# Kernel optimization log

Hardware: AMD Instinct MI355X
Metric: run time of the kernel (lower is better)

Reference implementation:

```python
import jax, jax.numpy as jnp
import numpy as np

TOP_P = 0.95        # sample() default topp
TEMPERATURE = 0.8   # token_temperature
NEG_INF = float('-inf')


def setup_inputs() -> dict:
    key = jax.random.key(0)
    k1, k2 = jax.random.split(key)
    B, V = 8192, 2048  # batch rows x speech-unit vocab
    logits = jax.random.normal(k1, (B, V), dtype=jnp.float32) * 4.0
    # uniform noise for Gumbel-max multinomial sampling (open interval)
    u = jax.random.uniform(k2, (B, V), dtype=jnp.float32, minval=1e-6, maxval=1.0 - 1e-6)
    return {"logits": logits, "u": u}


def _top_p_filter(logits, p):
    # descending sort (matches torch.sort(descending=True))
    order = jnp.argsort(-logits, axis=-1)                      # [B, V]
    sorted_logits = jnp.take_along_axis(logits, order, axis=-1)
    cum = jnp.cumsum(jax.nn.softmax(sorted_logits, axis=-1), axis=-1)
    remove = cum > p
    # shift right by one so the first token above the threshold is kept
    remove = jnp.concatenate(
        [jnp.zeros_like(remove[..., :1]), remove[..., :-1]], axis=-1)
    # scatter mask back to unsorted order via inverse permutation
    inv = jnp.argsort(order, axis=-1)
    remove_unsorted = jnp.take_along_axis(remove, inv, axis=-1)
    return jnp.where(remove_unsorted, NEG_INF, logits)


def reference(logits, u):
    scaled = logits / TEMPERATURE
    filtered = _top_p_filter(scaled, TOP_P)                    # [B, V]
    probs = jax.nn.softmax(filtered, axis=-1)                  # [B, V]
    # multinomial(probs, 1) == Gumbel-max over filtered logits
    gumbel = -jnp.log(-jnp.log(u))
    sampled = jnp.argmax(filtered + gumbel, axis=-1, keepdims=True)  # [B, 1]
    return sampled, probs
```

## Files before the change

### kernel.cpp

```cpp
#include <hip/hip_runtime.h>
#include <math.h>

#define VOCAB 2048
#define TPB   256
#define NBINS 64
#define BIN_SCALE 6.0f
#define BCAP  512

typedef float vf4 __attribute__((ext_vector_type(4)));

__device__ __forceinline__ unsigned long long pack_key(float z, int idx) {
    unsigned zb = __float_as_uint(z);
    zb = (zb & 0x80000000u) ? ~zb : (zb | 0x80000000u);
    return ((unsigned long long)zb << 32) | (unsigned)(VOCAB - 1 - idx);
}

__global__ __launch_bounds__(TPB, 8) void sampler_kernel(
    const float* __restrict__ logits,
    const float* __restrict__ uni,
    float* __restrict__ out_idx,
    float* __restrict__ out_probs)
{
    const int row  = blockIdx.x;
    const int t    = threadIdx.x;
    const int lane = t & 63;
    const int wid  = t >> 6;

    __shared__ float  s_bins[NBINS];
    __shared__ float  s_wf[4];
    __shared__ double s_wd[4];
    __shared__ unsigned long long s_key[4];
    __shared__ int    s_cnt;
    __shared__ float  s_cv[BCAP];
    __shared__ float  s_ce[BCAP];

    const float* lrow = logits    + (size_t)row * VOCAB;
    const float* urow = uni       + (size_t)row * VOCAB;
    float*       prow = out_probs + (size_t)row * VOCAB;

    if (t < NBINS) s_bins[t] = 0.0f;
    if (t == 0) s_cnt = 0;

    const vf4 a0 = *(const vf4*)(lrow + 4 * t);
    const vf4 a1 = *(const vf4*)(lrow + VOCAB / 2 + 4 * t);
    float s[8] = {a0.x * 1.25f, a0.y * 1.25f, a0.z * 1.25f, a0.w * 1.25f,
                  a1.x * 1.25f, a1.y * 1.25f, a1.z * 1.25f, a1.w * 1.25f};

    float lm = s[0];
    #pragma unroll
    for (int j = 1; j < 8; j++) lm = fmaxf(lm, s[j]);
    #pragma unroll
    for (int off = 32; off; off >>= 1) lm = fmaxf(lm, __shfl_down(lm, off));
    if (lane == 0) s_wf[wid] = lm;
    __syncthreads();
    const float m = fmaxf(fmaxf(s_wf[0], s_wf[1]), fmaxf(s_wf[2], s_wf[3]));

    float e[8];
    int   bin[8];
    float psum = 0.0f;
    #pragma unroll
    for (int j = 0; j < 8; j++) {
        e[j] = __expf(s[j] - m);
        psum += e[j];
        bin[j] = (int)((m - s[j]) * BIN_SCALE);
        if (bin[j] < NBINS) atomicAdd(&s_bins[bin[j]], e[j]);
    }
    double dp = (double)psum;
    #pragma unroll
    for (int off = 32; off; off >>= 1) dp += __shfl_down(dp, off);
    if (lane == 0) s_wd[wid] = dp;
    __syncthreads();

    const double S  = s_wd[0] + s_wd[1] + s_wd[2] + s_wd[3];
    const double pS = 0.95 * S;
    const float  bf = s_bins[lane];
    double c = (double)bf;
    #pragma unroll
    for (int d = 1; d < 64; d <<= 1) {
        double o = __shfl_up(c, d);
        if (lane >= d) c += o;
    }
    unsigned long long ball = __ballot(c > pS);
    const int    bstar     = ball ? (__ffsll(ball) - 1) : (NBINS - 1);
    const double cumBefore = __shfl(c - (double)bf, bstar);

    #pragma unroll
    for (int j = 0; j < 8; j++) {
        if (bin[j] == bstar) {
            int pos = atomicAdd(&s_cnt, 1);
            if (pos < BCAP) { s_cv[pos] = s[j]; s_ce[pos] = e[j]; }
        }
    }
    __syncthreads();
    const int cnt = min(s_cnt, BCAP);

    float SKb = 0.0f;
    for (int i = 0; i < cnt; i++) {
        float vi = s_cv[i], part = 0.0f;
        for (int jj = 0; jj < cnt; jj++)
            part += (s_cv[jj] > vi) ? s_ce[jj] : 0.0f;
        if (cumBefore + (double)part <= pS) SKb += s_ce[i];
    }
    const float invSK = 1.0f / (float)(cumBefore + (double)SKb);

    unsigned keptMask = 0;
    #pragma unroll
    for (int j = 0; j < 8; j++) {
        bool kept;
        if (bin[j] < bstar)      kept = true;
        else if (bin[j] > bstar) kept = false;
        else {
            float part = 0.0f;
            for (int i = 0; i < cnt; i++)
                part += (s_cv[i] > s[j]) ? s_ce[i] : 0.0f;
            kept = (cumBefore + (double)part) <= pS;
        }
        if (kept) keptMask |= (1u << j);
    }

    vf4 p0, p1;
    p0.x = (keptMask & 0x01) ? e[0] * invSK : 0.0f;
    p0.y = (keptMask & 0x02) ? e[1] * invSK : 0.0f;
    p0.z = (keptMask & 0x04) ? e[2] * invSK : 0.0f;
    p0.w = (keptMask & 0x08) ? e[3] * invSK : 0.0f;
    p1.x = (keptMask & 0x10) ? e[4] * invSK : 0.0f;
    p1.y = (keptMask & 0x20) ? e[5] * invSK : 0.0f;
    p1.z = (keptMask & 0x40) ? e[6] * invSK : 0.0f;
    p1.w = (keptMask & 0x80) ? e[7] * invSK : 0.0f;
    __builtin_nontemporal_store(p0, (vf4*)(prow + 4 * t));
    __builtin_nontemporal_store(p1, (vf4*)(prow + VOCAB / 2 + 4 * t));

    unsigned long long key = 0ull;
    #pragma unroll
    for (int j = 0; j < 8; j++) {
        if ((keptMask >> j) & 1u) {
            int   idx = (j < 4) ? (4 * t + j) : (VOCAB / 2 + 4 * t + (j - 4));
            float uv  = urow[idx];
            float z   = s[j] + (-logf(-logf(uv)));
            unsigned long long kk = pack_key(z, idx);
            key = (kk > key) ? kk : key;
        }
    }
    #pragma unroll
    for (int off = 32; off; off >>= 1) {
        unsigned long long ok = __shfl_down(key, off);
        key = (ok > key) ? ok : key;
    }
    if (lane == 0) s_key[wid] = key;
    __syncthreads();
    if (t == 0) {
        unsigned long long k0 = s_key[0];
        #pragma unroll
        for (int w = 1; w < 4; w++) k0 = (s_key[w] > k0) ? s_key[w] : k0;
        out_idx[row] = (float)(VOCAB - 1 - (int)(k0 & 0xFFFFFFFFu));
    }
}

extern "C" void kernel_launch(void* const* d_in, const int* in_sizes, int n_in,
                              void* d_out, int out_size, void* d_ws, size_t ws_size,
                              hipStream_t stream) {
    const float* logits = (const float*)d_in[0];
    const float* u      = (const float*)d_in[1];
    const int B = in_sizes[0] / VOCAB;
    float* out_idx   = (float*)d_out;
    float* out_probs = (float*)d_out + B;
    sampler_kernel<<<B, TPB, 0, stream>>>(logits, u, out_idx, out_probs);
}
```

Before: 183.8 us.

## Process one row per wavefront and compact kept tokens before Gumbel sampling

```diff
diff --git a/kernel.cpp b/kernel.cpp
--- a/kernel.cpp
+++ b/kernel.cpp
@@ -3,9 +3,12 @@
 
 #define VOCAB 2048
 #define TPB   256
+#define RPB   4
+#define EPT   32
+#define NCH   8
 #define NBINS 64
 #define BIN_SCALE 6.0f
-#define BCAP  512
+#define BCAP  256
 
 typedef float vf4 __attribute__((ext_vector_type(4)));
 
@@ -15,65 +18,66 @@
     return ((unsigned long long)zb << 32) | (unsigned)(VOCAB - 1 - idx);
 }
 
-__global__ __launch_bounds__(TPB, 8) void sampler_kernel(
+__global__ __launch_bounds__(TPB, 6) void sampler_kernel(
     const float* __restrict__ logits,
     const float* __restrict__ uni,
     float* __restrict__ out_idx,
     float* __restrict__ out_probs)
 {
-    const int row  = blockIdx.x;
-    const int t    = threadIdx.x;
-    const int lane = t & 63;
-    const int wid  = t >> 6;
+    const int wid  = threadIdx.x >> 6;
+    const int lane = threadIdx.x & 63;
+    const int row  = blockIdx.x * RPB + wid;
 
-    __shared__ float  s_bins[NBINS];
-    __shared__ float  s_wf[4];
-    __shared__ double s_wd[4];
-    __shared__ unsigned long long s_key[4];
-    __shared__ int    s_cnt;
-    __shared__ float  s_cv[BCAP];
-    __shared__ float  s_ce[BCAP];
+    __shared__ float s_bins[RPB][NBINS];
+    __shared__ float s_cv[RPB][BCAP];
+    __shared__ float s_ce[RPB][BCAP];
+    __shared__ int   s_cnt[RPB], s_cnt2[RPB];
+
+    float* bins = s_bins[wid];
+    float* cv   = s_cv[wid];
+    float* ce   = s_ce[wid];
 
     const float* lrow = logits    + (size_t)row * VOCAB;
     const float* urow = uni       + (size_t)row * VOCAB;
     float*       prow = out_probs + (size_t)row * VOCAB;
 
-    if (t < NBINS) s_bins[t] = 0.0f;
-    if (t == 0) s_cnt = 0;
+    bins[lane] = 0.0f;
+    if (lane == 0) { s_cnt[wid] = 0; s_cnt2[wid] = 0; }
+    __builtin_amdgcn_wave_barrier();
 
-    const vf4 a0 = *(const vf4*)(lrow + 4 * t);
-    const vf4 a1 = *(const vf4*)(lrow + VOCAB / 2 + 4 * t);
-    float s[8] = {a0.x * 1.25f, a0.y * 1.25f, a0.z * 1.25f, a0.w * 1.25f,
-                  a1.x * 1.25f, a1.y * 1.25f, a1.z * 1.25f, a1.w * 1.25f};
+    vf4 a[NCH];
+    #pragma unroll
+    for (int c = 0; c < NCH; c++)
+        a[c] = *(const vf4*)(lrow + c * 256 + lane * 4);
 
-    float lm = s[0];
+    float s[EPT];
     #pragma unroll
-    for (int j = 1; j < 8; j++) lm = fmaxf(lm, s[j]);
+    for (int c = 0; c < NCH; c++) {
+        s[4*c+0] = a[c].x * 1.25f; s[4*c+1] = a[c].y * 1.25f;
+        s[4*c+2] = a[c].z * 1.25f; s[4*c+3] = a[c].w * 1.25f;
+    }
+
+    float m = s[0];
     #pragma unroll
-    for (int off = 32; off; off >>= 1) lm = fmaxf(lm, __shfl_down(lm, off));
-    if (lane == 0) s_wf[wid] = lm;
-    __syncthreads();
-    const float m = fmaxf(fmaxf(s_wf[0], s_wf[1]), fmaxf(s_wf[2], s_wf[3]));
+    for (int j = 1; j < EPT; j++) m = fmaxf(m, s[j]);
+    #pragma unroll
+    for (int off = 32; off; off >>= 1) m = fmaxf(m, __shfl_xor(m, off));
 
-    float e[8];
-    int   bin[8];
     float psum = 0.0f;
     #pragma unroll
-    for (int j = 0; j < 8; j++) {
-        e[j] = __expf(s[j] - m);
-        psum += e[j];
-        bin[j] = (int)((m - s[j]) * BIN_SCALE);
-        if (bin[j] < NBINS) atomicAdd(&s_bins[bin[j]], e[j]);
+    for (int j = 0; j < EPT; j++) {
+        float e = __expf(s[j] - m);
+        psum += e;
+        int b = (int)((m - s[j]) * BIN_SCALE);
+        if (b < NBINS) atomicAdd(&bins[b], e);
     }
-    double dp = (double)psum;
+    double S = (double)psum;
     #pragma unroll
-    for (int off = 32; off; off >>= 1) dp += __shfl_down(dp, off);
-    if (lane == 0) s_wd[wid] = dp;
-    __syncthreads();
+    for (int off = 32; off; off >>= 1) S += __shfl_xor(S, off);
+    const double pS = 0.95 * S;
+    __builtin_amdgcn_wave_barrier();
 
-    const double S  = s_wd[0] + s_wd[1] + s_wd[2] + s_wd[3];
-    const double pS = 0.95 * S;
-    const float  bf = s_bins[lane];
+    const float bf = bins[lane];
     double c = (double)bf;
     #pragma unroll
     for (int d = 1; d < 64; d <<= 1) {
@@ -85,75 +89,84 @@
     const double cumBefore = __shfl(c - (double)bf, bstar);
 
     #pragma unroll
-    for (int j = 0; j < 8; j++) {
-        if (bin[j] == bstar) {
-            int pos = atomicAdd(&s_cnt, 1);
-            if (pos < BCAP) { s_cv[pos] = s[j]; s_ce[pos] = e[j]; }
+    for (int j = 0; j < EPT; j++) {
+        int b = (int)((m - s[j]) * BIN_SCALE);
+        if (b == bstar) {
+            int pos = atomicAdd(&s_cnt[wid], 1);
+            if (pos < BCAP) { cv[pos] = s[j]; ce[pos] = __expf(s[j] - m); }
         }
     }
-    __syncthreads();
-    const int cnt = min(s_cnt, BCAP);
+    __builtin_amdgcn_wave_barrier();
+    const int cnt = min(s_cnt[wid], BCAP);
 
     float SKb = 0.0f;
     for (int i = 0; i < cnt; i++) {
-        float vi = s_cv[i], part = 0.0f;
+        float vi = cv[i], part = 0.0f;
         for (int jj = 0; jj < cnt; jj++)
-            part += (s_cv[jj] > vi) ? s_ce[jj] : 0.0f;
-        if (cumBefore + (double)part <= pS) SKb += s_ce[i];
+            part += (cv[jj] > vi) ? ce[jj] : 0.0f;
+        if (cumBefore + (double)part <= pS) SKb += ce[i];
     }
     const float invSK = 1.0f / (float)(cumBefore + (double)SKb);
 
     unsigned keptMask = 0;
     #pragma unroll
-    for (int j = 0; j < 8; j++) {
+    for (int j = 0; j < EPT; j++) {
+        int  b = (int)((m - s[j]) * BIN_SCALE);
         bool kept;
-        if (bin[j] < bstar)      kept = true;
-        else if (bin[j] > bstar) kept = false;
+        if (b < bstar)      kept = true;
+        else if (b > bstar) kept = false;
         else {
             float part = 0.0f;
             for (int i = 0; i < cnt; i++)
-                part += (s_cv[i] > s[j]) ? s_ce[i] : 0.0f;
+                part += (cv[i] > s[j]) ? ce[i] : 0.0f;
             kept = (cumBefore + (double)part) <= pS;
         }
         if (kept) keptMask |= (1u << j);
     }
 
-    vf4 p0, p1;
-    p0.x = (keptMask & 0x01) ? e[0] * invSK : 0.0f;
-    p0.y = (keptMask & 0x02) ? e[1] * invSK : 0.0f;
-    p0.z = (keptMask & 0x04) ? e[2] * invSK : 0.0f;
-    p0.w = (keptMask & 0x08) ? e[3] * invSK : 0.0f;
-    p1.x = (keptMask & 0x10) ? e[4] * invSK : 0.0f;
-    p1.y = (keptMask & 0x20) ? e[5] * invSK : 0.0f;
-    p1.z = (keptMask & 0x40) ? e[6] * invSK : 0.0f;
-    p1.w = (keptMask & 0x80) ? e[7] * invSK : 0.0f;
-    __builtin_nontemporal_store(p0, (vf4*)(prow + 4 * t));
-    __builtin_nontemporal_store(p1, (vf4*)(prow + VOCAB / 2 + 4 * t));
+    #pragma unroll
+    for (int cch = 0; cch < NCH; cch++) {
+        vf4 p;
+        p.x = ((keptMask >> (4*cch+0)) & 1u) ? __expf(s[4*cch+0] - m) * invSK : 0.0f;
+        p.y = ((keptMask >> (4*cch+1)) & 1u) ? __expf(s[4*cch+1] - m) * invSK : 0.0f;
+        p.z = ((keptMask >> (4*cch+2)) & 1u) ? __expf(s[4*cch+2] - m) * invSK : 0.0f;
+        p.w = ((keptMask >> (4*cch+3)) & 1u) ? __expf(s[4*cch+3] - m) * invSK : 0.0f;
+        __builtin_nontemporal_store(p, (vf4*)(prow + cch * 256 + lane * 4));
+    }
+    __builtin_amdgcn_wave_barrier();
 
     unsigned long long key = 0ull;
     #pragma unroll
-    for (int j = 0; j < 8; j++) {
+    for (int j = 0; j < EPT; j++) {
         if ((keptMask >> j) & 1u) {
-            int   idx = (j < 4) ? (4 * t + j) : (VOCAB / 2 + 4 * t + (j - 4));
-            float uv  = urow[idx];
-            float z   = s[j] + (-logf(-logf(uv)));
-            unsigned long long kk = pack_key(z, idx);
-            key = (kk > key) ? kk : key;
+            int idx = (j >> 2) * 256 + lane * 4 + (j & 3);
+            int pos = atomicAdd(&s_cnt2[wid], 1);
+            if (pos < BCAP) { cv[pos] = s[j]; ce[pos] = __int_as_float(idx); }
+            else {
+                float z = s[j] + (-logf(-logf(urow[idx])));
+                unsigned long long kk = pack_key(z, idx);
+                key = (kk > key) ? kk : key;
+            }
         }
+    }
+    __builtin_amdgcn_wave_barrier();
+    const int k  = s_cnt2[wid];
+    const int kl = min(k, BCAP);
+
+    for (int i = lane; i < kl; i += 64) {
+        float sv  = cv[i];
+        int   idx = __float_as_int(ce[i]);
+        float z   = sv + (-logf(-logf(urow[idx])));
+        unsigned long long kk = pack_key(z, idx);
+        key = (kk > key) ? kk : key;
     }
     #pragma unroll
     for (int off = 32; off; off >>= 1) {
-        unsigned long long ok = __shfl_down(key, off);
+        unsigned long long ok = __shfl_xor(key, off);
         key = (ok > key) ? ok : key;
     }
-    if (lane == 0) s_key[wid] = key;
-    __syncthreads();
-    if (t == 0) {
-        unsigned long long k0 = s_key[0];
-        #pragma unroll
-        for (int w = 1; w < 4; w++) k0 = (s_key[w] > k0) ? s_key[w] : k0;
-        out_idx[row] = (float)(VOCAB - 1 - (int)(k0 & 0xFFFFFFFFu));
-    }
+    if (lane == 0)
+        out_idx[row] = (float)(VOCAB - 1 - (int)(key & 0xFFFFFFFFu));
 }
 
 extern "C" void kernel_launch(void* const* d_in, const int* in_sizes, int n_in,
@@ -164,5 +177,5 @@
     const int B = in_sizes[0] / VOCAB;
     float* out_idx   = (float*)d_out;
     float* out_probs = (float*)d_out + B;
-    sampler_kernel<<<B, TPB, 0, stream>>>(logits, u, out_idx, out_probs);
+    sampler_kernel<<<B / RPB, TPB, 0, stream>>>(logits, u, out_idx, out_probs);
 }
```

Result: slower. 237.8 us (+29.4%).
